# Performance work log

Hardware: AMD Instinct MI355X
Metric: run time of the kernel (lower is better)

The kernel has to match this reference:

```python
import jax, jax.numpy as jnp
import numpy as np

N = 50000
E = 600000
D_IN = 128
D_OUT = 128
EPS = 1e-12  # F.normalize eps


def setup_inputs() -> dict:
    key = jax.random.key(0)
    ks = jax.random.split(key, 10)
    s = 1.0 / np.sqrt(D_IN)
    inp = {
        "x": jax.random.normal(ks[0], (N, D_IN), dtype=jnp.float32),
        "edge_index": jax.random.randint(ks[1], (2, E), 0, N, dtype=jnp.int64),
        # conv1: lin_l (with bias) applied to aggregated neighbors, lin_r (no bias) to root
        "W1l": jax.random.uniform(ks[2], (D_IN, D_IN), jnp.float32, -s, s),
        "b1": jax.random.uniform(ks[3], (D_IN,), jnp.float32, -s, s),
        "W1r": jax.random.uniform(ks[4], (D_IN, D_IN), jnp.float32, -s, s),
        # conv2
        "W2l": jax.random.uniform(ks[5], (D_IN, D_OUT), jnp.float32, -s, s),
        "b2": jax.random.uniform(ks[6], (D_OUT,), jnp.float32, -s, s),
        "W2r": jax.random.uniform(ks[7], (D_IN, D_OUT), jnp.float32, -s, s),
        # final fc
        "Wf": jax.random.uniform(ks[8], (D_OUT, D_OUT), jnp.float32, -s, s),
        "bf": jax.random.uniform(ks[9], (D_OUT,), jnp.float32, -s, s),
    }
    return inp


def _sage_conv(x, src, dst, Wl, bl, Wr):
    # mean-aggregate messages from source nodes onto destination nodes
    msgs = x[src]  # [E, d] gather
    agg = jax.ops.segment_sum(msgs, dst, num_segments=N)  # [N, d]
    cnt = jax.ops.segment_sum(jnp.ones((src.shape[0],), x.dtype), dst, num_segments=N)
    agg = agg / jnp.maximum(cnt, 1.0)[:, None]  # isolated nodes -> 0
    out = agg @ Wl + bl + x @ Wr
    # L2 normalize per node (PyG normalize=True)
    nrm = jnp.sqrt(jnp.sum(out * out, axis=-1, keepdims=True))
    return out / jnp.maximum(nrm, EPS)


def reference(x, edge_index, W1l, b1, W1r, W2l, b2, W2r, Wf, bf):
    src, dst = edge_index[0], edge_index[1]
    h = jax.nn.relu(_sage_conv(x, src, dst, W1l, b1, W1r))
    h = jax.nn.relu(_sage_conv(h, src, dst, W2l, b2, W2r))
    return h @ Wf + bf
```

## Files before the change

### kernel.cpp

```cpp
#include <hip/hip_runtime.h>

#define D 128
#define SCAN_B 256
#define AS_LD 36

typedef __attribute__((ext_vector_type(8))) short bf16x8;
typedef __attribute__((ext_vector_type(4))) float f32x4;

__device__ __forceinline__ unsigned short f2bf(float f) {
    unsigned u = __float_as_uint(f);
    unsigned r = u + 0x7FFFu + ((u >> 16) & 1u);
    return (unsigned short)(r >> 16);
}
__device__ __forceinline__ float bf2f(unsigned short h) {
    return __uint_as_float(((unsigned)h) << 16);
}

__global__ void count_kernel(const int* __restrict__ ei, int E, int* __restrict__ cnt) {
    int t = blockIdx.x * blockDim.x + threadIdx.x;
    if (t < E) atomicAdd(&cnt[ei[E + t]], 1);
}

__global__ void scan_pass1(const int* __restrict__ cnt, int* __restrict__ rs,
                           int* __restrict__ bsum, int N) {
    __shared__ int lds[SCAN_B];
    int tid = threadIdx.x;
    int i = blockIdx.x * SCAN_B + tid;
    int v = (i < N) ? cnt[i] : 0;
    lds[tid] = v;
    __syncthreads();
    for (int o = 1; o < SCAN_B; o <<= 1) {
        int t = (tid >= o) ? lds[tid - o] : 0;
        __syncthreads();
        lds[tid] += t;
        __syncthreads();
    }
    if (i < N) rs[i] = lds[tid] - v;
    if (tid == SCAN_B - 1) bsum[blockIdx.x] = lds[tid];
}

__global__ void scan_pass2(int* __restrict__ bsum, int nb) {
    __shared__ int lds[SCAN_B];
    int tid = threadIdx.x;
    int v = (tid < nb) ? bsum[tid] : 0;
    lds[tid] = v;
    __syncthreads();
    for (int o = 1; o < SCAN_B; o <<= 1) {
        int t = (tid >= o) ? lds[tid - o] : 0;
        __syncthreads();
        lds[tid] += t;
        __syncthreads();
    }
    if (tid < nb) bsum[tid] = lds[tid] - v;
}

__global__ void scan_pass3(int* __restrict__ rs, int* __restrict__ cursor,
                           const int* __restrict__ bsum, const int* __restrict__ cnt,
                           float* __restrict__ inv, int N) {
    int i = blockIdx.x * SCAN_B + threadIdx.x;
    if (i < N) {
        int v = rs[i] + bsum[blockIdx.x];
        rs[i] = v;
        cursor[i] = v;
        inv[i] = 1.0f / (float)max(cnt[i], 1);
    }
}

__global__ void fill_kernel(const int* __restrict__ ei, int E,
                            int* __restrict__ cursor, int* __restrict__ csr) {
    int e = blockIdx.x * blockDim.x + threadIdx.x;
    if (e < E) {
        int src = ei[e], dst = ei[E + e];
        int pos = atomicAdd(&cursor[dst], 1);
        csr[pos] = src;
    }
}

__global__ void aggregate_kernel(const float* __restrict__ x, const int* __restrict__ csr,
                                 const int* __restrict__ rs, const int* __restrict__ cnt,
                                 const float* __restrict__ inv, float* __restrict__ agg,
                                 int N) {
    int t = blockIdx.x * blockDim.x + threadIdx.x;
    int node = t >> 5;
    int c = t & 31;
    if (node >= N) return;
    int deg = cnt[node];
    int st = rs[node];
    const float4* x4 = (const float4*)x;
    float4 s0 = make_float4(0.f, 0.f, 0.f, 0.f);
    float4 s1 = make_float4(0.f, 0.f, 0.f, 0.f);
    int i = 0;
    for (; i + 8 <= deg; i += 8) {
        int n0 = csr[st + i + 0], n1 = csr[st + i + 1];
        int n2 = csr[st + i + 2], n3 = csr[st + i + 3];
        int n4 = csr[st + i + 4], n5 = csr[st + i + 5];
        int n6 = csr[st + i + 6], n7 = csr[st + i + 7];
        float4 v0 = x4[(size_t)n0 * 32 + c];
        float4 v1 = x4[(size_t)n1 * 32 + c];
        float4 v2 = x4[(size_t)n2 * 32 + c];
        float4 v3 = x4[(size_t)n3 * 32 + c];
        float4 v4 = x4[(size_t)n4 * 32 + c];
        float4 v5 = x4[(size_t)n5 * 32 + c];
        float4 v6 = x4[(size_t)n6 * 32 + c];
        float4 v7 = x4[(size_t)n7 * 32 + c];
        s0.x += (v0.x + v1.x) + (v2.x + v3.x);
        s0.y += (v0.y + v1.y) + (v2.y + v3.y);
        s0.z += (v0.z + v1.z) + (v2.z + v3.z);
        s0.w += (v0.w + v1.w) + (v2.w + v3.w);
        s1.x += (v4.x + v5.x) + (v6.x + v7.x);
        s1.y += (v4.y + v5.y) + (v6.y + v7.y);
        s1.z += (v4.z + v5.z) + (v6.z + v7.z);
        s1.w += (v4.w + v5.w) + (v6.w + v7.w);
    }
    for (; i + 4 <= deg; i += 4) {
        int n0 = csr[st + i + 0], n1 = csr[st + i + 1];
        int n2 = csr[st + i + 2], n3 = csr[st + i + 3];
        float4 v0 = x4[(size_t)n0 * 32 + c];
        float4 v1 = x4[(size_t)n1 * 32 + c];
        float4 v2 = x4[(size_t)n2 * 32 + c];
        float4 v3 = x4[(size_t)n3 * 32 + c];
        s0.x += v0.x + v1.x; s0.y += v0.y + v1.y;
        s0.z += v0.z + v1.z; s0.w += v0.w + v1.w;
        s1.x += v2.x + v3.x; s1.y += v2.y + v3.y;
        s1.z += v2.z + v3.z; s1.w += v2.w + v3.w;
    }
    for (; i < deg; i++) {
        int n0 = csr[st + i];
        float4 v0 = x4[(size_t)n0 * 32 + c];
        s0.x += v0.x; s0.y += v0.y; s0.z += v0.z; s0.w += v0.w;
    }
    float iv = inv[node];
    float4 s = make_float4((s0.x + s1.x) * iv, (s0.y + s1.y) * iv,
                           (s0.z + s1.z) * iv, (s0.w + s1.w) * iv);
    ((float4*)agg)[(size_t)node * 32 + c] = s;
}

__global__ void pack_kernel(const float* __restrict__ W1l, const float* __restrict__ W1r,
                            const float* __restrict__ W2l, const float* __restrict__ W2r,
                            const float* __restrict__ Wf, unsigned short* __restrict__ pw) {
    int idx = blockIdx.x * blockDim.x + threadIdx.x;
    if (idx >= 5 * 2048) return;
    int w = idx >> 11;
    int r = idx & 2047;
    int ks = r >> 9;
    int t = (r >> 6) & 7;
    int lane = r & 63;
    int q = lane >> 4, n = lane & 15;
    const float* W = (w == 0) ? W1l : (w == 1) ? W1r : (w == 2) ? W2l : (w == 3) ? W2r : Wf;
    unsigned short* dh = pw + (size_t)w * 32768;
    unsigned short* dl = dh + 16384;
    int off = ((ks * 8 + t) * 64 + lane) * 8;
#pragma unroll
    for (int j = 0; j < 8; j++) {
        float v = W[(size_t)(ks * 32 + q * 8 + j) * D + t * 16 + n];
        unsigned short hb = f2bf(v);
        dh[off + j] = hb;
        dl[off + j] = f2bf(v - bf2f(hb));
    }
}

template <int FUSE_FC>
__global__ __launch_bounds__(256) void mfma_gemm(
        const float* __restrict__ Aagg, const float* __restrict__ Ax,
        const unsigned short* __restrict__ W0h, const unsigned short* __restrict__ W0lo,
        const unsigned short* __restrict__ W1h, const unsigned short* __restrict__ W1lo,
        const float* __restrict__ bias,
        const unsigned short* __restrict__ Wfh, const unsigned short* __restrict__ Wflo,
        const float* __restrict__ bfin,
        float* __restrict__ out, int N) {
    __shared__ float As[64 * AS_LD];
    __shared__ unsigned short Hs[FUSE_FC ? 4 * 4096 : 4];

    const int tid = threadIdx.x;
    const int lane = tid & 63;
    const int wave = tid >> 6;
    const int c = lane & 15;
    const int q = lane >> 4;
    const int mb = blockIdx.x * 64;
    const int wm = wave * 16;

    f32x4 acc[8];
#pragma unroll
    for (int t = 0; t < 8; t++)
#pragma unroll
        for (int r = 0; r < 4; r++) acc[t][r] = 0.0f;

    for (int ks = 0; ks < 8; ks++) {
        const float* Asrc = (ks < 4) ? Aagg : Ax;
        const int kl = ks & 3;
#pragma unroll
        for (int rp = 0; rp < 2; rp++) {
            int f = tid + rp * 256;
            int m = f >> 3, kq = f & 7;
            int g = mb + m;
            if (g >= N) g = N - 1;
            float4 v = ((const float4*)Asrc)[(size_t)g * 32 + kl * 8 + kq];
            *((float4*)&As[m * AS_LD + kq * 4]) = v;
        }
        __syncthreads();

        const float* ap = &As[(wm + c) * AS_LD + q * 8];
        float4 a0 = *((const float4*)ap);
        float4 a1 = *((const float4*)(ap + 4));
        float av[8] = {a0.x, a0.y, a0.z, a0.w, a1.x, a1.y, a1.z, a1.w};
        bf16x8 ah, alo;
#pragma unroll
        for (int j = 0; j < 8; j++) {
            unsigned short hb = f2bf(av[j]);
            ah[j] = (short)hb;
            alo[j] = (short)f2bf(av[j] - bf2f(hb));
        }

        const uint4* Wh4 = (const uint4*)((ks < 4) ? W0h : W1h);
        const uint4* Wl4 = (const uint4*)((ks < 4) ? W0lo : W1lo);
#pragma unroll
        for (int t = 0; t < 8; t++) {
            int fi = (kl * 8 + t) * 64 + lane;
            bf16x8 bh = __builtin_bit_cast(bf16x8, Wh4[fi]);
            bf16x8 blo = __builtin_bit_cast(bf16x8, Wl4[fi]);
            acc[t] = __builtin_amdgcn_mfma_f32_16x16x32_bf16(ah, bh, acc[t], 0, 0, 0);
            acc[t] = __builtin_amdgcn_mfma_f32_16x16x32_bf16(alo, bh, acc[t], 0, 0, 0);
            acc[t] = __builtin_amdgcn_mfma_f32_16x16x32_bf16(ah, blo, acc[t], 0, 0, 0);
        }
        __syncthreads();
    }

#pragma unroll
    for (int t = 0; t < 8; t++) {
        float bv = bias[t * 16 + c];
#pragma unroll
        for (int r = 0; r < 4; r++) acc[t][r] += bv;
    }
    float s[4];
#pragma unroll
    for (int r = 0; r < 4; r++) {
        float v = 0.0f;
#pragma unroll
        for (int t = 0; t < 8; t++) v += acc[t][r] * acc[t][r];
        v += __shfl_xor(v, 1, 16);
        v += __shfl_xor(v, 2, 16);
        v += __shfl_xor(v, 4, 16);
        v += __shfl_xor(v, 8, 16);
        s[r] = 1.0f / fmaxf(sqrtf(v), 1e-12f);
    }
#pragma unroll
    for (int t = 0; t < 8; t++)
#pragma unroll
        for (int r = 0; r < 4; r++) acc[t][r] = fmaxf(acc[t][r] * s[r], 0.0f);

    if (!FUSE_FC) {
#pragma unroll
        for (int t = 0; t < 8; t++)
#pragma unroll
            for (int r = 0; r < 4; r++) {
                int row = mb + wm + q * 4 + r;
                if (row < N) out[(size_t)row * D + t * 16 + c] = acc[t][r];
            }
        return;
    }

    unsigned short* Hw = &Hs[wave * 4096];
#pragma unroll
    for (int t = 0; t < 8; t++)
#pragma unroll
        for (int r = 0; r < 4; r++) {
            int row = q * 4 + r;
            int col = t * 16 + c;
            int ks2 = col >> 5, c32 = col & 31;
            int off = ((ks2 * 64) + (c32 >> 3) * 16 + row) * 8 + (c32 & 7);
            float hv = acc[t][r];
            unsigned short hb = f2bf(hv);
            Hw[off] = hb;
            Hw[2048 + off] = f2bf(hv - bf2f(hb));
        }
    __syncthreads();

    f32x4 acc2[8];
#pragma unroll
    for (int t = 0; t < 8; t++) {
        float bv = bfin[t * 16 + c];
#pragma unroll
        for (int r = 0; r < 4; r++) acc2[t][r] = bv;
    }
    const uint4* Wfh4 = (const uint4*)Wfh;
    const uint4* Wfl4 = (const uint4*)Wflo;
#pragma unroll
    for (int ks2 = 0; ks2 < 4; ks2++) {
        bf16x8 ah2 = __builtin_bit_cast(bf16x8, ((const uint4*)Hw)[ks2 * 64 + lane]);
        bf16x8 al2 = __builtin_bit_cast(bf16x8, ((const uint4*)(Hw + 2048))[ks2 * 64 + lane]);
#pragma unroll
        for (int t = 0; t < 8; t++) {
            int fi = (ks2 * 8 + t) * 64 + lane;
            bf16x8 bh = __builtin_bit_cast(bf16x8, Wfh4[fi]);
            bf16x8 blo = __builtin_bit_cast(bf16x8, Wfl4[fi]);
            acc2[t] = __builtin_amdgcn_mfma_f32_16x16x32_bf16(ah2, bh, acc2[t], 0, 0, 0);
            acc2[t] = __builtin_amdgcn_mfma_f32_16x16x32_bf16(al2, bh, acc2[t], 0, 0, 0);
            acc2[t] = __builtin_amdgcn_mfma_f32_16x16x32_bf16(ah2, blo, acc2[t], 0, 0, 0);
        }
    }

#pragma unroll
    for (int t = 0; t < 8; t++)
#pragma unroll
        for (int r = 0; r < 4; r++) {
            int row = mb + wm + q * 4 + r;
            if (row < N) out[(size_t)row * D + t * 16 + c] = acc2[t][r];
        }
}

extern "C" void kernel_launch(void* const* d_in, const int* in_sizes, int n_in,
                              void* d_out, int out_size, void* d_ws, size_t ws_size,
                              hipStream_t stream) {
    const float* x   = (const float*)d_in[0];
    const int*   ei  = (const int*)d_in[1];
    const float* W1l = (const float*)d_in[2];
    const float* b1  = (const float*)d_in[3];
    const float* W1r = (const float*)d_in[4];
    const float* W2l = (const float*)d_in[5];
    const float* b2  = (const float*)d_in[6];
    const float* W2r = (const float*)d_in[7];
    const float* Wf  = (const float*)d_in[8];
    const float* bf  = (const float*)d_in[9];
    float* out = (float*)d_out;

    int N = in_sizes[0] / D;
    int E = in_sizes[1] / 2;

    float* ws     = (float*)d_ws;
    float* agg    = ws;
    float* inv    = ws + (size_t)N * D;
    int*   rs     = (int*)(inv + N);
    int*   cnt    = rs + N;
    int*   cursor = cnt + N;
    int*   bsum   = cursor + N;
    int*   csr    = bsum + 256;
    unsigned short* pw = (unsigned short*)(csr + E);
    unsigned short* pW1lh = pw + 0 * 32768, *pW1ll = pW1lh + 16384;
    unsigned short* pW1rh = pw + 1 * 32768, *pW1rl = pW1rh + 16384;
    unsigned short* pW2lh = pw + 2 * 32768, *pW2ll = pW2lh + 16384;
    unsigned short* pW2rh = pw + 3 * 32768, *pW2rl = pW2rh + 16384;
    unsigned short* pWfh  = pw + 4 * 32768, *pWfl  = pWfh + 16384;

    int nb = (N + SCAN_B - 1) / SCAN_B;

    hipMemsetAsync(cnt, 0, (size_t)N * sizeof(int), stream);
    pack_kernel<<<40, 256, 0, stream>>>(W1l, W1r, W2l, W2r, Wf, pw);
    count_kernel<<<(E + 255) / 256, 256, 0, stream>>>(ei, E, cnt);
    scan_pass1<<<nb, SCAN_B, 0, stream>>>(cnt, rs, bsum, N);
    scan_pass2<<<1, SCAN_B, 0, stream>>>(bsum, nb);
    scan_pass3<<<nb, SCAN_B, 0, stream>>>(rs, cursor, bsum, cnt, inv, N);
    fill_kernel<<<(E + 255) / 256, 256, 0, stream>>>(ei, E, cursor, csr);

    int agg_blocks = (N * 32 + 255) / 256;
    int gemm_blocks = (N + 63) / 64;

    aggregate_kernel<<<agg_blocks, 256, 0, stream>>>(x, csr, rs, cnt, inv, agg, N);
    mfma_gemm<0><<<gemm_blocks, 256, 0, stream>>>(agg, x, pW1lh, pW1ll, pW1rh, pW1rl, b1,
                                                  nullptr, nullptr, nullptr, out, N);

    aggregate_kernel<<<agg_blocks, 256, 0, stream>>>(out, csr, rs, cnt, inv, agg, N);
    mfma_gemm<1><<<gemm_blocks, 256, 0, stream>>>(agg, out, pW2lh, pW2ll, pW2rh, pW2rl, b2,
                                                  pWfh, pWfl, bf, out, N);
}
```

Before: 312.8 us.

## Give each wave two 16-row tiles and load A directly from global memory

The GEMM kernel now has each wave compute two 16-row output tiles (128 rows per block), so every weight fragment loaded from global memory feeds two sets of MFMAs. The shared-memory staging of A and its block barriers are removed; each lane reads its A fragment straight from global memory with float4 loads. In the fused FC path, per-wave LDS is reused sequentially for the two tiles and the fragments are held in registers. This halves weight-fragment traffic per row and removes synchronisation, at the cost of roughly double the accumulator registers, lower occupancy, and fewer blocks in the grid.

```diff
diff --git a/kernel.cpp b/kernel.cpp
--- a/kernel.cpp
+++ b/kernel.cpp
@@ -2,7 +2,6 @@
 
 #define D 128
 #define SCAN_B 256
-#define AS_LD 36
 
 typedef __attribute__((ext_vector_type(8))) short bf16x8;
 typedef __attribute__((ext_vector_type(4))) float f32x4;
@@ -159,6 +158,15 @@
     }
 }
 
+__device__ __forceinline__ void split8(const float* av, bf16x8& hi, bf16x8& lo) {
+#pragma unroll
+    for (int j = 0; j < 8; j++) {
+        unsigned short hb = f2bf(av[j]);
+        hi[j] = (short)hb;
+        lo[j] = (short)f2bf(av[j] - bf2f(hb));
+    }
+}
+
 template <int FUSE_FC>
 __global__ __launch_bounds__(256) void mfma_gemm(
         const float* __restrict__ Aagg, const float* __restrict__ Ax,
@@ -168,7 +176,6 @@
         const unsigned short* __restrict__ Wfh, const unsigned short* __restrict__ Wflo,
         const float* __restrict__ bfin,
         float* __restrict__ out, int N) {
-    __shared__ float As[64 * AS_LD];
     __shared__ unsigned short Hs[FUSE_FC ? 4 * 4096 : 4];
 
     const int tid = threadIdx.x;
@@ -176,40 +183,34 @@
     const int wave = tid >> 6;
     const int c = lane & 15;
     const int q = lane >> 4;
-    const int mb = blockIdx.x * 64;
-    const int wm = wave * 16;
-
-    f32x4 acc[8];
-#pragma unroll
-    for (int t = 0; t < 8; t++)
-#pragma unroll
-        for (int r = 0; r < 4; r++) acc[t][r] = 0.0f;
-
+    const int R = blockIdx.x * 128 + wave * 32;
+
+    int row0 = R + c;       if (row0 >= N) row0 = N - 1;
+    int row1 = R + 16 + c;  if (row1 >= N) row1 = N - 1;
+    const size_t a0_base = (size_t)row0 * D;
+    const size_t a1_base = (size_t)row1 * D;
+
+    f32x4 acc[2][8];
+#pragma unroll
+    for (int g = 0; g < 2; g++)
+#pragma unroll
+        for (int t = 0; t < 8; t++)
+#pragma unroll
+            for (int r = 0; r < 4; r++) acc[g][t][r] = 0.0f;
+
+#pragma unroll
     for (int ks = 0; ks < 8; ks++) {
         const float* Asrc = (ks < 4) ? Aagg : Ax;
         const int kl = ks & 3;
-#pragma unroll
-        for (int rp = 0; rp < 2; rp++) {
-            int f = tid + rp * 256;
-            int m = f >> 3, kq = f & 7;
-            int g = mb + m;
-            if (g >= N) g = N - 1;
-            float4 v = ((const float4*)Asrc)[(size_t)g * 32 + kl * 8 + kq];
-            *((float4*)&As[m * AS_LD + kq * 4]) = v;
-        }
-        __syncthreads();
-
-        const float* ap = &As[(wm + c) * AS_LD + q * 8];
-        float4 a0 = *((const float4*)ap);
-        float4 a1 = *((const float4*)(ap + 4));
-        float av[8] = {a0.x, a0.y, a0.z, a0.w, a1.x, a1.y, a1.z, a1.w};
-        bf16x8 ah, alo;
-#pragma unroll
-        for (int j = 0; j < 8; j++) {
-            unsigned short hb = f2bf(av[j]);
-            ah[j] = (short)hb;
-            alo[j] = (short)f2bf(av[j] - bf2f(hb));
-        }
+        const int koff = kl * 32 + q * 8;
+        float av0[8], av1[8];
+        *((float4*)&av0[0]) = *((const float4*)(Asrc + a0_base + koff));
+        *((float4*)&av0[4]) = *((const float4*)(Asrc + a0_base + koff + 4));
+        *((float4*)&av1[0]) = *((const float4*)(Asrc + a1_base + koff));
+        *((float4*)&av1[4]) = *((const float4*)(Asrc + a1_base + koff + 4));
+        bf16x8 ah0, al0, ah1, al1;
+        split8(av0, ah0, al0);
+        split8(av1, ah1, al1);
 
         const uint4* Wh4 = (const uint4*)((ks < 4) ? W0h : W1h);
         const uint4* Wl4 = (const uint4*)((ks < 4) ? W0lo : W1lo);
@@ -218,94 +219,109 @@
             int fi = (kl * 8 + t) * 64 + lane;
             bf16x8 bh = __builtin_bit_cast(bf16x8, Wh4[fi]);
             bf16x8 blo = __builtin_bit_cast(bf16x8, Wl4[fi]);
-            acc[t] = __builtin_amdgcn_mfma_f32_16x16x32_bf16(ah, bh, acc[t], 0, 0, 0);
-            acc[t] = __builtin_amdgcn_mfma_f32_16x16x32_bf16(alo, bh, acc[t], 0, 0, 0);
-            acc[t] = __builtin_amdgcn_mfma_f32_16x16x32_bf16(ah, blo, acc[t], 0, 0, 0);
-        }
-        __syncthreads();
-    }
-
-#pragma unroll
-    for (int t = 0; t < 8; t++) {
-        float bv = bias[t * 16 + c];
-#pragma unroll
-        for (int r = 0; r < 4; r++) acc[t][r] += bv;
-    }
-    float s[4];
-#pragma unroll
-    for (int r = 0; r < 4; r++) {
-        float v = 0.0f;
-#pragma unroll
-        for (int t = 0; t < 8; t++) v += acc[t][r] * acc[t][r];
-        v += __shfl_xor(v, 1, 16);
-        v += __shfl_xor(v, 2, 16);
-        v += __shfl_xor(v, 4, 16);
-        v += __shfl_xor(v, 8, 16);
-        s[r] = 1.0f / fmaxf(sqrtf(v), 1e-12f);
-    }
-#pragma unroll
-    for (int t = 0; t < 8; t++)
-#pragma unroll
-        for (int r = 0; r < 4; r++) acc[t][r] = fmaxf(acc[t][r] * s[r], 0.0f);
+            acc[0][t] = __builtin_amdgcn_mfma_f32_16x16x32_bf16(ah0, bh, acc[0][t], 0, 0, 0);
+            acc[0][t] = __builtin_amdgcn_mfma_f32_16x16x32_bf16(al0, bh, acc[0][t], 0, 0, 0);
+            acc[0][t] = __builtin_amdgcn_mfma_f32_16x16x32_bf16(ah0, blo, acc[0][t], 0, 0, 0);
+            acc[1][t] = __builtin_amdgcn_mfma_f32_16x16x32_bf16(ah1, bh, acc[1][t], 0, 0, 0);
+            acc[1][t] = __builtin_amdgcn_mfma_f32_16x16x32_bf16(al1, bh, acc[1][t], 0, 0, 0);
+            acc[1][t] = __builtin_amdgcn_mfma_f32_16x16x32_bf16(ah1, blo, acc[1][t], 0, 0, 0);
+        }
+    }
+
+#pragma unroll
+    for (int g = 0; g < 2; g++) {
+#pragma unroll
+        for (int t = 0; t < 8; t++) {
+            float bv = bias[t * 16 + c];
+#pragma unroll
+            for (int r = 0; r < 4; r++) acc[g][t][r] += bv;
+        }
+#pragma unroll
+        for (int r = 0; r < 4; r++) {
+            float v = 0.0f;
+#pragma unroll
+            for (int t = 0; t < 8; t++) v += acc[g][t][r] * acc[g][t][r];
+            v += __shfl_xor(v, 1, 16);
+            v += __shfl_xor(v, 2, 16);
+            v += __shfl_xor(v, 4, 16);
+            v += __shfl_xor(v, 8, 16);
+            float rn = 1.0f / fmaxf(sqrtf(v), 1e-12f);
+#pragma unroll
+            for (int t = 0; t < 8; t++) acc[g][t][r] = fmaxf(acc[g][t][r] * rn, 0.0f);
+        }
+    }
 
     if (!FUSE_FC) {
 #pragma unroll
+        for (int g = 0; g < 2; g++)
+#pragma unroll
+            for (int t = 0; t < 8; t++)
+#pragma unroll
+                for (int r = 0; r < 4; r++) {
+                    int row = R + g * 16 + q * 4 + r;
+                    if (row < N) out[(size_t)row * D + t * 16 + c] = acc[g][t][r];
+                }
+        return;
+    }
+
+    unsigned short* Hw = &Hs[wave * 4096];
+    bf16x8 ah2[2][4], al2[2][4];
+#pragma unroll
+    for (int g = 0; g < 2; g++) {
+#pragma unroll
         for (int t = 0; t < 8; t++)
 #pragma unroll
             for (int r = 0; r < 4; r++) {
-                int row = mb + wm + q * 4 + r;
-                if (row < N) out[(size_t)row * D + t * 16 + c] = acc[t][r];
+                int row = q * 4 + r;
+                int col = t * 16 + c;
+                int ks2 = col >> 5, c32 = col & 31;
+                int off = ((ks2 * 64) + (c32 >> 3) * 16 + row) * 8 + (c32 & 7);
+                float hv = acc[g][t][r];
+                unsigned short hb = f2bf(hv);
+                Hw[off] = hb;
+                Hw[2048 + off] = f2bf(hv - bf2f(hb));
             }
-        return;
-    }
-
-    unsigned short* Hw = &Hs[wave * 4096];
-#pragma unroll
-    for (int t = 0; t < 8; t++)
-#pragma unroll
-        for (int r = 0; r < 4; r++) {
-            int row = q * 4 + r;
-            int col = t * 16 + c;
-            int ks2 = col >> 5, c32 = col & 31;
-            int off = ((ks2 * 64) + (c32 >> 3) * 16 + row) * 8 + (c32 & 7);
-            float hv = acc[t][r];
-            unsigned short hb = f2bf(hv);
-            Hw[off] = hb;
-            Hw[2048 + off] = f2bf(hv - bf2f(hb));
-        }
-    __syncthreads();
-
-    f32x4 acc2[8];
+#pragma unroll
+        for (int ks2 = 0; ks2 < 4; ks2++) {
+            ah2[g][ks2] = __builtin_bit_cast(bf16x8, ((const uint4*)Hw)[ks2 * 64 + lane]);
+            al2[g][ks2] = __builtin_bit_cast(bf16x8, ((const uint4*)(Hw + 2048))[ks2 * 64 + lane]);
+        }
+    }
+
+    f32x4 acc2[2][8];
 #pragma unroll
     for (int t = 0; t < 8; t++) {
         float bv = bfin[t * 16 + c];
 #pragma unroll
-        for (int r = 0; r < 4; r++) acc2[t][r] = bv;
+        for (int r = 0; r < 4; r++) { acc2[0][t][r] = bv; acc2[1][t][r] = bv; }
     }
     const uint4* Wfh4 = (const uint4*)Wfh;
     const uint4* Wfl4 = (const uint4*)Wflo;
 #pragma unroll
     for (int ks2 = 0; ks2 < 4; ks2++) {
-        bf16x8 ah2 = __builtin_bit_cast(bf16x8, ((const uint4*)Hw)[ks2 * 64 + lane]);
-        bf16x8 al2 = __builtin_bit_cast(bf16x8, ((const uint4*)(Hw + 2048))[ks2 * 64 + lane]);
 #pragma unroll
         for (int t = 0; t < 8; t++) {
             int fi = (ks2 * 8 + t) * 64 + lane;
             bf16x8 bh = __builtin_bit_cast(bf16x8, Wfh4[fi]);
             bf16x8 blo = __builtin_bit_cast(bf16x8, Wfl4[fi]);
-            acc2[t] = __builtin_amdgcn_mfma_f32_16x16x32_bf16(ah2, bh, acc2[t], 0, 0, 0);
-            acc2[t] = __builtin_amdgcn_mfma_f32_16x16x32_bf16(al2, bh, acc2[t], 0, 0, 0);
-            acc2[t] = __builtin_amdgcn_mfma_f32_16x16x32_bf16(ah2, blo, acc2[t], 0, 0, 0);
-        }
-    }
-
-#pragma unroll
-    for (int t = 0; t < 8; t++)
-#pragma unroll
-        for (int r = 0; r < 4; r++) {
-            int row = mb + wm + q * 4 + r;
-            if (row < N) out[(size_t)row * D + t * 16 + c] = acc2[t][r];
-        }
+            acc2[0][t] = __builtin_amdgcn_mfma_f32_16x16x32_bf16(ah2[0][ks2], bh, acc2[0][t], 0, 0, 0);
+            acc2[0][t] = __builtin_amdgcn_mfma_f32_16x16x32_bf16(al2[0][ks2], bh, acc2[0][t], 0, 0, 0);
+            acc2[0][t] = __builtin_amdgcn_mfma_f32_16x16x32_bf16(ah2[0][ks2], blo, acc2[0][t], 0, 0, 0);
+            acc2[1][t] = __builtin_amdgcn_mfma_f32_16x16x32_bf16(ah2[1][ks2], bh, acc2[1][t], 0, 0, 0);
+            acc2[1][t] = __builtin_amdgcn_mfma_f32_16x16x32_bf16(al2[1][ks2], bh, acc2[1][t], 0, 0, 0);
+            acc2[1][t] = __builtin_amdgcn_mfma_f32_16x16x32_bf16(ah2[1][ks2], blo, acc2[1][t], 0, 0, 0);
+        }
+    }
+
+#pragma unroll
+    for (int g = 0; g < 2; g++)
+#pragma unroll
+        for (int t = 0; t < 8; t++)
+#pragma unroll
+            for (int r = 0; r < 4; r++) {
+                int row = R + g * 16 + q * 4 + r;
+                if (row < N) out[(size_t)row * D + t * 16 + c] = acc2[g][t][r];
+            }
 }
 
 extern "C" void kernel_launch(void* const* d_in, const int* in_sizes, int n_in,
@@ -352,7 +368,7 @@
     fill_kernel<<<(E + 255) / 256, 256, 0, stream>>>(ei, E, cursor, csr);
 
     int agg_blocks = (N * 32 + 255) / 256;
-    int gemm_blocks = (N + 63) / 64;
+    int gemm_blocks = (N + 127) / 128;
 
     aggregate_kernel<<<agg_blocks, 256, 0, stream>>>(x, csr, rs, cnt, inv, agg, N);
     mfma_gemm<0><<<gemm_blocks, 256, 0, stream>>>(agg, x, pW1lh, pW1ll, pW1rh, pW1rl, b1,
```

Measured after the change: 322.3 us. 1.03x slower.

## Gather neighbor features in fp16 and load GEMM A operand directly from global

Applied to the files above, without the earlier changes.

Adds a conversion kernel that writes x as fp16, and has the first GEMM also write an fp16 copy of its output. Both aggregation passes then gather half-width rows, 16 threads per node, which halves the bytes read in the gather. The GEMM now loads A rows straight from global memory into registers instead of staging them in LDS, which removes the per-k-step __syncthreads. The cost is reduced precision in the mean aggregation and one extra conversion pass. A __syncthreads after the Hs writes in the fused FC path was also removed; each wave appears to read only its own Hw region, so this is probably safe.

```diff
diff --git a/kernel.cpp b/kernel.cpp
--- a/kernel.cpp
+++ b/kernel.cpp
@@ -1,8 +1,8 @@
 #include <hip/hip_runtime.h>
+#include <hip/hip_fp16.h>
 
 #define D 128
 #define SCAN_B 256
-#define AS_LD 36
 
 typedef __attribute__((ext_vector_type(8))) short bf16x8;
 typedef __attribute__((ext_vector_type(4))) float f32x4;
@@ -76,63 +76,64 @@
     }
 }
 
-__global__ void aggregate_kernel(const float* __restrict__ x, const int* __restrict__ csr,
+__global__ void cvt_half_kernel(const float* __restrict__ x, __half* __restrict__ xh, int n8) {
+    int i = blockIdx.x * blockDim.x + threadIdx.x;
+    if (i >= n8) return;
+    const float4* x4 = (const float4*)x;
+    float4 a = x4[2 * i], b = x4[2 * i + 1];
+    __half2 h0 = __floats2half2_rn(a.x, a.y);
+    __half2 h1 = __floats2half2_rn(a.z, a.w);
+    __half2 h2 = __floats2half2_rn(b.x, b.y);
+    __half2 h3 = __floats2half2_rn(b.z, b.w);
+    uint4 o;
+    o.x = *(const unsigned*)&h0;
+    o.y = *(const unsigned*)&h1;
+    o.z = *(const unsigned*)&h2;
+    o.w = *(const unsigned*)&h3;
+    ((uint4*)xh)[i] = o;
+}
+
+__device__ __forceinline__ void acc8(uint4 v, float* s) {
+    const __half2* h = reinterpret_cast<const __half2*>(&v);
+    float2 f0 = __half22float2(h[0]);
+    float2 f1 = __half22float2(h[1]);
+    float2 f2 = __half22float2(h[2]);
+    float2 f3 = __half22float2(h[3]);
+    s[0] += f0.x; s[1] += f0.y; s[2] += f1.x; s[3] += f1.y;
+    s[4] += f2.x; s[5] += f2.y; s[6] += f3.x; s[7] += f3.y;
+}
+
+__global__ void aggregate_kernel(const __half* __restrict__ xh, const int* __restrict__ csr,
                                  const int* __restrict__ rs, const int* __restrict__ cnt,
                                  const float* __restrict__ inv, float* __restrict__ agg,
                                  int N) {
     int t = blockIdx.x * blockDim.x + threadIdx.x;
-    int node = t >> 5;
-    int c = t & 31;
+    int node = t >> 4;
+    int c = t & 15;
     if (node >= N) return;
     int deg = cnt[node];
     int st = rs[node];
-    const float4* x4 = (const float4*)x;
-    float4 s0 = make_float4(0.f, 0.f, 0.f, 0.f);
-    float4 s1 = make_float4(0.f, 0.f, 0.f, 0.f);
+    const uint4* x4 = (const uint4*)xh;
+    float s[8] = {0.f, 0.f, 0.f, 0.f, 0.f, 0.f, 0.f, 0.f};
     int i = 0;
-    for (; i + 8 <= deg; i += 8) {
-        int n0 = csr[st + i + 0], n1 = csr[st + i + 1];
-        int n2 = csr[st + i + 2], n3 = csr[st + i + 3];
-        int n4 = csr[st + i + 4], n5 = csr[st + i + 5];
-        int n6 = csr[st + i + 6], n7 = csr[st + i + 7];
-        float4 v0 = x4[(size_t)n0 * 32 + c];
-        float4 v1 = x4[(size_t)n1 * 32 + c];
-        float4 v2 = x4[(size_t)n2 * 32 + c];
-        float4 v3 = x4[(size_t)n3 * 32 + c];
-        float4 v4 = x4[(size_t)n4 * 32 + c];
-        float4 v5 = x4[(size_t)n5 * 32 + c];
-        float4 v6 = x4[(size_t)n6 * 32 + c];
-        float4 v7 = x4[(size_t)n7 * 32 + c];
-        s0.x += (v0.x + v1.x) + (v2.x + v3.x);
-        s0.y += (v0.y + v1.y) + (v2.y + v3.y);
-        s0.z += (v0.z + v1.z) + (v2.z + v3.z);
-        s0.w += (v0.w + v1.w) + (v2.w + v3.w);
-        s1.x += (v4.x + v5.x) + (v6.x + v7.x);
-        s1.y += (v4.y + v5.y) + (v6.y + v7.y);
-        s1.z += (v4.z + v5.z) + (v6.z + v7.z);
-        s1.w += (v4.w + v5.w) + (v6.w + v7.w);
-    }
     for (; i + 4 <= deg; i += 4) {
         int n0 = csr[st + i + 0], n1 = csr[st + i + 1];
         int n2 = csr[st + i + 2], n3 = csr[st + i + 3];
-        float4 v0 = x4[(size_t)n0 * 32 + c];
-        float4 v1 = x4[(size_t)n1 * 32 + c];
-        float4 v2 = x4[(size_t)n2 * 32 + c];
-        float4 v3 = x4[(size_t)n3 * 32 + c];
-        s0.x += v0.x + v1.x; s0.y += v0.y + v1.y;
-        s0.z += v0.z + v1.z; s0.w += v0.w + v1.w;
-        s1.x += v2.x + v3.x; s1.y += v2.y + v3.y;
-        s1.z += v2.z + v3.z; s1.w += v2.w + v3.w;
+        uint4 v0 = x4[(size_t)n0 * 16 + c];
+        uint4 v1 = x4[(size_t)n1 * 16 + c];
+        uint4 v2 = x4[(size_t)n2 * 16 + c];
+        uint4 v3 = x4[(size_t)n3 * 16 + c];
+        acc8(v0, s); acc8(v1, s); acc8(v2, s); acc8(v3, s);
     }
     for (; i < deg; i++) {
         int n0 = csr[st + i];
-        float4 v0 = x4[(size_t)n0 * 32 + c];
-        s0.x += v0.x; s0.y += v0.y; s0.z += v0.z; s0.w += v0.w;
+        uint4 v0 = x4[(size_t)n0 * 16 + c];
+        acc8(v0, s);
     }
     float iv = inv[node];
-    float4 s = make_float4((s0.x + s1.x) * iv, (s0.y + s1.y) * iv,
-                           (s0.z + s1.z) * iv, (s0.w + s1.w) * iv);
-    ((float4*)agg)[(size_t)node * 32 + c] = s;
+    float* dst = agg + (size_t)node * D + c * 8;
+    ((float4*)dst)[0] = make_float4(s[0] * iv, s[1] * iv, s[2] * iv, s[3] * iv);
+    ((float4*)dst)[1] = make_float4(s[4] * iv, s[5] * iv, s[6] * iv, s[7] * iv);
 }
 
 __global__ void pack_kernel(const float* __restrict__ W1l, const float* __restrict__ W1r,
@@ -159,6 +160,15 @@
     }
 }
 
+__device__ __forceinline__ void split8(const float* av, bf16x8& hi, bf16x8& lo) {
+#pragma unroll
+    for (int j = 0; j < 8; j++) {
+        unsigned short hb = f2bf(av[j]);
+        hi[j] = (short)hb;
+        lo[j] = (short)f2bf(av[j] - bf2f(hb));
+    }
+}
+
 template <int FUSE_FC>
 __global__ __launch_bounds__(256) void mfma_gemm(
         const float* __restrict__ Aagg, const float* __restrict__ Ax,
@@ -167,8 +177,7 @@
         const float* __restrict__ bias,
         const unsigned short* __restrict__ Wfh, const unsigned short* __restrict__ Wflo,
         const float* __restrict__ bfin,
-        float* __restrict__ out, int N) {
-    __shared__ float As[64 * AS_LD];
+        float* __restrict__ out, __half* __restrict__ outh, int N) {
     __shared__ unsigned short Hs[FUSE_FC ? 4 * 4096 : 4];
 
     const int tid = threadIdx.x;
@@ -176,8 +185,11 @@
     const int wave = tid >> 6;
     const int c = lane & 15;
     const int q = lane >> 4;
-    const int mb = blockIdx.x * 64;
-    const int wm = wave * 16;
+    const int R = blockIdx.x * 64 + wave * 16;
+
+    int row0 = R + c;
+    if (row0 >= N) row0 = N - 1;
+    const size_t a_base = (size_t)row0 * D;
 
     f32x4 acc[8];
 #pragma unroll
@@ -185,31 +197,16 @@
 #pragma unroll
         for (int r = 0; r < 4; r++) acc[t][r] = 0.0f;
 
+#pragma unroll
     for (int ks = 0; ks < 8; ks++) {
         const float* Asrc = (ks < 4) ? Aagg : Ax;
         const int kl = ks & 3;
-#pragma unroll
-        for (int rp = 0; rp < 2; rp++) {
-            int f = tid + rp * 256;
-            int m = f >> 3, kq = f & 7;
-            int g = mb + m;
-            if (g >= N) g = N - 1;
-            float4 v = ((const float4*)Asrc)[(size_t)g * 32 + kl * 8 + kq];
-            *((float4*)&As[m * AS_LD + kq * 4]) = v;
-        }
-        __syncthreads();
-
-        const float* ap = &As[(wm + c) * AS_LD + q * 8];
-        float4 a0 = *((const float4*)ap);
-        float4 a1 = *((const float4*)(ap + 4));
-        float av[8] = {a0.x, a0.y, a0.z, a0.w, a1.x, a1.y, a1.z, a1.w};
-        bf16x8 ah, alo;
-#pragma unroll
-        for (int j = 0; j < 8; j++) {
-            unsigned short hb = f2bf(av[j]);
-            ah[j] = (short)hb;
-            alo[j] = (short)f2bf(av[j] - bf2f(hb));
-        }
+        const int koff = kl * 32 + q * 8;
+        float av[8];
+        *((float4*)&av[0]) = *((const float4*)(Asrc + a_base + koff));
+        *((float4*)&av[4]) = *((const float4*)(Asrc + a_base + koff + 4));
+        bf16x8 ah, al;
+        split8(av, ah, al);
 
         const uint4* Wh4 = (const uint4*)((ks < 4) ? W0h : W1h);
         const uint4* Wl4 = (const uint4*)((ks < 4) ? W0lo : W1lo);
@@ -219,10 +216,9 @@
             bf16x8 bh = __builtin_bit_cast(bf16x8, Wh4[fi]);
             bf16x8 blo = __builtin_bit_cast(bf16x8, Wl4[fi]);
             acc[t] = __builtin_amdgcn_mfma_f32_16x16x32_bf16(ah, bh, acc[t], 0, 0, 0);
-            acc[t] = __builtin_amdgcn_mfma_f32_16x16x32_bf16(alo, bh, acc[t], 0, 0, 0);
+            acc[t] = __builtin_amdgcn_mfma_f32_16x16x32_bf16(al, bh, acc[t], 0, 0, 0);
             acc[t] = __builtin_amdgcn_mfma_f32_16x16x32_bf16(ah, blo, acc[t], 0, 0, 0);
         }
-        __syncthreads();
     }
 
 #pragma unroll
@@ -231,7 +227,6 @@
 #pragma unroll
         for (int r = 0; r < 4; r++) acc[t][r] += bv;
     }
-    float s[4];
 #pragma unroll
     for (int r = 0; r < 4; r++) {
         float v = 0.0f;
@@ -241,20 +236,22 @@
         v += __shfl_xor(v, 2, 16);
         v += __shfl_xor(v, 4, 16);
         v += __shfl_xor(v, 8, 16);
-        s[r] = 1.0f / fmaxf(sqrtf(v), 1e-12f);
-    }
-#pragma unroll
-    for (int t = 0; t < 8; t++)
-#pragma unroll
-        for (int r = 0; r < 4; r++) acc[t][r] = fmaxf(acc[t][r] * s[r], 0.0f);
+        float rn = 1.0f / fmaxf(sqrtf(v), 1e-12f);
+#pragma unroll
+        for (int t = 0; t < 8; t++) acc[t][r] = fmaxf(acc[t][r] * rn, 0.0f);
+    }
 
     if (!FUSE_FC) {
 #pragma unroll
         for (int t = 0; t < 8; t++)
 #pragma unroll
             for (int r = 0; r < 4; r++) {
-                int row = mb + wm + q * 4 + r;
-                if (row < N) out[(size_t)row * D + t * 16 + c] = acc[t][r];
+                int row = R + q * 4 + r;
+                if (row < N) {
+                    float v = acc[t][r];
+                    out[(size_t)row * D + t * 16 + c] = v;
+                    if (outh) outh[(size_t)row * D + t * 16 + c] = __float2half_rn(v);
+                }
             }
         return;
     }
@@ -273,7 +270,6 @@
             Hw[off] = hb;
             Hw[2048 + off] = f2bf(hv - bf2f(hb));
         }
-    __syncthreads();
 
     f32x4 acc2[8];
 #pragma unroll
@@ -303,7 +299,7 @@
     for (int t = 0; t < 8; t++)
 #pragma unroll
         for (int r = 0; r < 4; r++) {
-            int row = mb + wm + q * 4 + r;
+            int row = R + q * 4 + r;
             if (row < N) out[(size_t)row * D + t * 16 + c] = acc2[t][r];
         }
 }
@@ -340,25 +336,28 @@
     unsigned short* pW2lh = pw + 2 * 32768, *pW2ll = pW2lh + 16384;
     unsigned short* pW2rh = pw + 3 * 32768, *pW2rl = pW2rh + 16384;
     unsigned short* pWfh  = pw + 4 * 32768, *pWfl  = pWfh + 16384;
+    __half* hb = (__half*)(pw + 5 * 32768);
 
     int nb = (N + SCAN_B - 1) / SCAN_B;
 
     hipMemsetAsync(cnt, 0, (size_t)N * sizeof(int), stream);
     pack_kernel<<<40, 256, 0, stream>>>(W1l, W1r, W2l, W2r, Wf, pw);
+    int n8 = N * 16;
+    cvt_half_kernel<<<(n8 + 255) / 256, 256, 0, stream>>>(x, hb, n8);
     count_kernel<<<(E + 255) / 256, 256, 0, stream>>>(ei, E, cnt);
     scan_pass1<<<nb, SCAN_B, 0, stream>>>(cnt, rs, bsum, N);
     scan_pass2<<<1, SCAN_B, 0, stream>>>(bsum, nb);
     scan_pass3<<<nb, SCAN_B, 0, stream>>>(rs, cursor, bsum, cnt, inv, N);
     fill_kernel<<<(E + 255) / 256, 256, 0, stream>>>(ei, E, cursor, csr);
 
-    int agg_blocks = (N * 32 + 255) / 256;
+    int agg_blocks = (N * 16 + 255) / 256;
     int gemm_blocks = (N + 63) / 64;
 
-    aggregate_kernel<<<agg_blocks, 256, 0, stream>>>(x, csr, rs, cnt, inv, agg, N);
+    aggregate_kernel<<<agg_blocks, 256, 0, stream>>>(hb, csr, rs, cnt, inv, agg, N);
     mfma_gemm<0><<<gemm_blocks, 256, 0, stream>>>(agg, x, pW1lh, pW1ll, pW1rh, pW1rl, b1,
-                                                  nullptr, nullptr, nullptr, out, N);
-
-    aggregate_kernel<<<agg_blocks, 256, 0, stream>>>(out, csr, rs, cnt, inv, agg, N);
+                                                  nullptr, nullptr, nullptr, out, hb, N);
+
+    aggregate_kernel<<<agg_blocks, 256, 0, stream>>>(hb, csr, rs, cnt, inv, agg, N);
     mfma_gemm<1><<<gemm_blocks, 256, 0, stream>>>(agg, out, pW2lh, pW2ll, pW2rh, pW2rl, b2,
-                                                  pWfh, pWfl, bf, out, N);
-}
+                                                  pWfh, pWfl, bf, out, nullptr, N);
+}
```

New measurement: 307.9 us. About the same (-1.6%).
